# Performance work log

Measured on AMD Instinct MI355X. Metric: run time of the kernel, lower is better.

The kernel has to match this reference:

```python
import jax, jax.numpy as jnp
import numpy as np


def _build_skew(coeff, gate, left, right):
    # coeff: [B, r], gate: [B], left/right: [F, r]
    scaled_left = left[None, :, :] * coeff[:, None, :]          # [B, F, r]
    base = jnp.einsum('bfr,gr->bfg', scaled_left, right)         # [B, F, F]
    skew = base - jnp.swapaxes(base, -1, -2)
    return gate[:, None, None] * skew


def setup_inputs() -> dict:
    key = jax.random.key(0)
    ks = jax.random.split(key, 10)
    B, N, F, R = 8, 4096, 512, 16
    return {
        'x': jax.random.normal(ks[0], (B, N, F), dtype=jnp.float32),
        'coeff': jax.random.normal(ks[1], (B, R), dtype=jnp.float32),
        'gate': jax.random.uniform(ks[2], (B,), dtype=jnp.float32),
        'coeff_local': jax.random.normal(ks[3], (B, R), dtype=jnp.float32),
        'gate_local': jax.random.uniform(ks[4], (B,), dtype=jnp.float32),
        'comm_scale': jax.random.uniform(ks[5], (B,), dtype=jnp.float32),
        'left': jax.random.normal(ks[6], (F, R), dtype=jnp.float32) / np.sqrt(F),
        'right': jax.random.normal(ks[7], (F, R), dtype=jnp.float32) / np.sqrt(F),
        'left_local': jax.random.normal(ks[8], (F, R), dtype=jnp.float32) / np.sqrt(F),
        'right_local': jax.random.normal(ks[9], (F, R), dtype=jnp.float32) / np.sqrt(F),
    }


def reference(x, coeff, gate, coeff_local, gate_local, comm_scale,
              left, right, left_local, right_local):
    F_dim = left.shape[0]
    global_skew = _build_skew(coeff, gate, left, right)                  # [B, F, F]
    local_skew = _build_skew(coeff_local, gate_local, left_local, right_local)
    omega = 0.5 * (global_skew + local_skew)
    commutator = local_skew @ global_skew - global_skew @ local_skew
    omega = omega + comm_scale[:, None, None] * (commutator / 12.0)
    eye = jnp.eye(F_dim, dtype=jnp.float32)[None, :, :]
    # Cayley transform: (I - 0.5*Omega)^{-1} (I + 0.5*Omega)
    transform = jnp.linalg.solve(eye - 0.5 * omega, eye + 0.5 * omega)   # [B, F, F]
    mixed = jnp.einsum('bnd,bdh->bnh', x, transform)
    return mixed.astype(x.dtype)
```

## Files before the change

kernel.cpp:

```cpp
#include <hip/hip_runtime.h>

#define B_ 8
#define N_ 4096
#define F_ 512

typedef __attribute__((ext_vector_type(8))) short bf16x8;
typedef __attribute__((ext_vector_type(4))) float f32x4;

#define XPAD 524

__device__ __forceinline__ float Sval(const float* l, const float* r,
                                      const float* ll, const float* rl,
                                      int h, int e) {
    const int m = e >> 4, c = e & 15;
    const float* p = (m == 0) ? l : (m == 1) ? r : (m == 2) ? ll : rl;
    return p[h * 16 + c];
}

__device__ __forceinline__ float qval(const float* coeff, const float* coeff_l,
                                      int b, int j) {
    if (j < 16) return 1.f;
    if (j < 32) return coeff[b * 16 + (j - 16)];
    if (j < 48) return 1.f;
    return coeff_l[b * 16 + (j - 48)];
}

__device__ __forceinline__ float lane_bcast(float v, int lane) {
    return __int_as_float(__builtin_amdgcn_readlane(__float_as_int(v), lane));
}

__device__ __forceinline__ unsigned short bf16_rn(float x) {
    unsigned u = __float_as_uint(x);
    unsigned r = u + 0x7FFFu + ((u >> 16) & 1u);
    return (unsigned short)(r >> 16);
}

__device__ __forceinline__ void bf16_split(float x, short& hi, short& lo) {
    const unsigned short h = bf16_rn(x);
    const float hf = __uint_as_float(((unsigned)h) << 16);
    const unsigned short s = bf16_rn(x - hf);
    hi = (short)h; lo = (short)s;
}

__device__ __forceinline__ float b2f(unsigned short u) {
    return __uint_as_float(((unsigned)u) << 16);
}

__global__ __launch_bounds__(256) void k_prep(const float* l, const float* r,
                                              const float* ll, const float* rl,
                                              float* GS, unsigned short* Sf) {
    __shared__ float red[4][64];
    const int i = blockIdx.x;
    const int t = threadIdx.x;
    const int j = t & 63, seg = t >> 6;

    {
        const int ht = i >> 1, eh = i & 1;
        for (int idx = t; idx < 512; idx += 256) {
            const int lx = idx >> 3, ii = idx & 7;
            const int h = ht * 16 + (lx & 15);
            const int e = eh * 32 + ((lx >> 4) & 3) * 8 + ii;
            short hh, ss;
            bf16_split(Sval(l, r, ll, rl, h, e), hh, ss);
            Sf[(i * 2 + 0) * 512 + idx] = (unsigned short)hh;
            Sf[(i * 2 + 1) * 512 + idx] = (unsigned short)ss;
        }
    }

    float acc = 0.f;
    const int h0 = seg * 128;
    for (int h = h0; h < h0 + 128; ++h)
        acc += Sval(l, r, ll, rl, h, i) * Sval(l, r, ll, rl, h, j);
    red[seg][j] = acc;
    __syncthreads();
    if (t < 64) GS[i * 64 + t] = red[0][t] + red[1][t] + red[2][t] + red[3][t];
}

__global__ __launch_bounds__(256) void k_pre(const float* coeff, const float* gate,
                                             const float* coeff_l, const float* gate_l,
                                             const float* comm, const float* GS,
                                             float* Mws, float* CPws) {
    __shared__ float GST[4096];
    __shared__ float CPs[4096];
    __shared__ float ABs[2048];
    __shared__ float u1s[32], u2s[32];

    const int b = blockIdx.x, t = threadIdx.x;
    const int tx = t & 15, ty = t >> 4;
    const float g = gate[b], gl = gate_l[b];
    const float cs = comm[b] / 12.0f;

    if (t < 32) {
        u1s[t] = (t < 16) ? g * coeff[b * 16 + t] : -g;
        u2s[t] = (t < 16) ? gl * coeff_l[b * 16 + t] : -gl;
    }
    for (int idx = t; idx < 4096; idx += 256) {
        const int i = idx & 63, e = idx >> 6;
        GST[idx] = -0.5f * qval(coeff, coeff_l, b, i) * GS[(i ^ 16) * 64 + e];
    }
    __syncthreads();

    for (int idx = t; idx < 2048; idx += 256) {
        const int which = idx >> 10;
        const int i = (idx >> 5) & 31, j = idx & 31;
        float val;
        if (which == 0) {
            const int v2i = (i < 16) ? 48 + i : 16 + i;
            const float v2sc = (i < 16) ? 1.f : coeff_l[b * 16 + (i - 16)];
            val = v2sc * u1s[j] * GS[v2i * 64 + j];
        } else {
            const int v1i = (i < 16) ? 16 + i : i - 16;
            const float v1sc = (i < 16) ? 1.f : coeff[b * 16 + (i - 16)];
            val = v1sc * u2s[j] * GS[v1i * 64 + 32 + j];
        }
        ABs[idx] = val;
    }
    __syncthreads();

    for (int idx = t; idx < 4096; idx += 256) {
        const int e = idx >> 6, j = idx & 63;
        float val = 0.f;
        if (j < 32) {
            if (e == j) val += 0.5f * u1s[j];
            if (e >= 32) val += cs * u2s[e - 32] * ABs[(e - 32) * 32 + j];
        } else {
            const int jp = j - 32;
            if (e == 32 + jp) val += 0.5f * u2s[jp];
            if (e < 32) val -= cs * u1s[e] * ABs[1024 + e * 32 + jp];
        }
        CPs[idx] = val;
        CPws[b * 4096 + idx] = val;
    }
    __syncthreads();

    {
        const int i0 = ty * 4, m0 = tx * 4;
        float acc[4][4];
#pragma unroll
        for (int i = 0; i < 4; ++i)
#pragma unroll
            for (int j = 0; j < 4; ++j) acc[i][j] = 0.f;
        for (int e = 0; e < 64; ++e) {
            const float4 av = *reinterpret_cast<const float4*>(&GST[e * 64 + i0]);
            const float4 bv = *reinterpret_cast<const float4*>(&CPs[e * 64 + m0]);
            const float a[4] = {av.x, av.y, av.z, av.w};
            const float bb[4] = {bv.x, bv.y, bv.z, bv.w};
#pragma unroll
            for (int i = 0; i < 4; ++i)
#pragma unroll
                for (int j = 0; j < 4; ++j) acc[i][j] += a[i] * bb[j];
        }
#pragma unroll
        for (int i = 0; i < 4; ++i) {
            float4 o;
            o.x = acc[i][0] + (((i0 + i) == (m0 + 0)) ? 1.f : 0.f);
            o.y = acc[i][1] + (((i0 + i) == (m0 + 1)) ? 1.f : 0.f);
            o.z = acc[i][2] + (((i0 + i) == (m0 + 2)) ? 1.f : 0.f);
            o.w = acc[i][3] + (((i0 + i) == (m0 + 3)) ? 1.f : 0.f);
            *reinterpret_cast<float4*>(&Mws[b * 4096 + (i0 + i) * 64 + m0]) = o;
        }
    }
}

#define DO64(M, K) \
    M(0, K) M(1, K) M(2, K) M(3, K) M(4, K) M(5, K) M(6, K) M(7, K) \
    M(8, K) M(9, K) M(10, K) M(11, K) M(12, K) M(13, K) M(14, K) M(15, K) \
    M(16, K) M(17, K) M(18, K) M(19, K) M(20, K) M(21, K) M(22, K) M(23, K) \
    M(24, K) M(25, K) M(26, K) M(27, K) M(28, K) M(29, K) M(30, K) M(31, K) \
    M(32, K) M(33, K) M(34, K) M(35, K) M(36, K) M(37, K) M(38, K) M(39, K) \
    M(40, K) M(41, K) M(42, K) M(43, K) M(44, K) M(45, K) M(46, K) M(47, K) \
    M(48, K) M(49, K) M(50, K) M(51, K) M(52, K) M(53, K) M(54, K) M(55, K) \
    M(56, K) M(57, K) M(58, K) M(59, K) M(60, K) M(61, K) M(62, K) M(63, K)

#define GJ_LOAD(RR, K) a[RR] = Mws[base + (RR)*64 + t];
#define GJ_STORE(RR, K) Kws[base + (RR)*64 + t] = a[RR];

#define INV_SNAP(RR, G) if (ing) Msnap[(RR) * 8 + gl] = a[RR];

#define IGU(I, G, J) \
    if ((I) != (J)) { \
        const float f_ = lane_bcast(a[(G)*8 + (I)], (G)*8 + (J)); \
        a[(G)*8 + (I)] = __builtin_fmaf(-f_, akp[J], a[(G)*8 + (I)]); \
    }

#define IGS(G, J) { \
    const float dk = lane_bcast(a[(G)*8 + (J)], (G)*8 + (J)); \
    const float pinv = 1.0f / dk; \
    a[(G)*8 + (J)] = (t == ((G)*8 + (J))) ? pinv : a[(G)*8 + (J)] * pinv; \
    akp[J] = a[(G)*8 + (J)] + ((t == ((G)*8 + (J))) ? 1.0f : 0.0f); \
    IGU(0, G, J) IGU(1, G, J) IGU(2, G, J) IGU(3, G, J) \
    IGU(4, G, J) IGU(5, G, J) IGU(6, G, J) IGU(7, G, J) }

#define TRL(RR, G) \
    if (((RR) >> 3) != (G)) { \
        const float4 m0 = *reinterpret_cast<const float4*>(&Msnap[(RR) * 8]); \
        const float4 m1 = *reinterpret_cast<const float4*>(&Msnap[(RR) * 8 + 4]); \
        a[RR] = __builtin_fmaf(-m0.x, akp[0], a[RR]); \
        a[RR] = __builtin_fmaf(-m0.y, akp[1], a[RR]); \
        a[RR] = __builtin_fmaf(-m0.z, akp[2], a[RR]); \
        a[RR] = __builtin_fmaf(-m0.w, akp[3], a[RR]); \
        a[RR] = __builtin_fmaf(-m1.x, akp[4], a[RR]); \
        a[RR] = __builtin_fmaf(-m1.y, akp[5], a[RR]); \
        a[RR] = __builtin_fmaf(-m1.z, akp[6], a[RR]); \
        a[RR] = __builtin_fmaf(-m1.w, akp[7], a[RR]); \
    }

#define MACRO_STEP(G) { \
    float akp[8]; \
    const bool ing = ((t >> 3) == (G)); \
    DO64(INV_SNAP, G) \
    IGS(G, 0) IGS(G, 1) IGS(G, 2) IGS(G, 3) \
    IGS(G, 4) IGS(G, 5) IGS(G, 6) IGS(G, 7) \
    DO64(TRL, G) }

__global__ __launch_bounds__(64, 1) void k_inv(const float* Mws, float* Kws) {
    __shared__ float Msnap[512];
    const int b = blockIdx.x, t = threadIdx.x;
    const int base = b * 4096;
    const int gl = t & 7;
    float a[64];
    DO64(GJ_LOAD, 0)
    MACRO_STEP(0) MACRO_STEP(1) MACRO_STEP(2) MACRO_STEP(3)
    MACRO_STEP(4) MACRO_STEP(5) MACRO_STEP(6) MACRO_STEP(7)
    DO64(GJ_STORE, 0)
}

__global__ __launch_bounds__(256) void k_sepost(const float* coeff, const float* coeff_l,
                                                const float* l, const float* r,
                                                const float* ll, const float* rl,
                                                const float* Mws, const float* CPws,
                                                const float* Kws, unsigned short* SEf) {
    __shared__ float smem[20480];
    float* Ms  = smem;
    float* CPs = smem + 4096;
    float* Ks  = smem + 8192;
    float* Tds = smem + 12288;
    float* Tas = smem + 16384;
    float* Es  = smem;
    float* Ss  = smem + 4096;
    float* SEs = smem + 8320;

    const int b = blockIdx.y, hc = blockIdx.x, t = threadIdx.x;
    const int tx = t & 15, ty = t >> 4;

    for (int idx = t; idx < 4096; idx += 256) {
        Ms[idx] = Mws[b * 4096 + idx];
        CPs[idx] = CPws[b * 4096 + idx];
        Ks[idx] = Kws[b * 4096 + idx];
    }
    __syncthreads();

    {
        const int i0 = ty * 4, j0 = tx * 4;
        float accd[4][4], acca[4][4];
#pragma unroll
        for (int i = 0; i < 4; ++i)
#pragma unroll
            for (int j = 0; j < 4; ++j) { accd[i][j] = 0.f; acca[i][j] = 0.f; }
        for (int q = 0; q < 64; ++q) {
            const float4 bv = *reinterpret_cast<const float4*>(&Ks[q * 64 + j0]);
            const float bb[4] = {bv.x, bv.y, bv.z, bv.w};
            float ad[4], aa[4];
#pragma unroll
            for (int i = 0; i < 4; ++i) {
                ad[i] = CPs[(i0 + i) * 64 + q];
                aa[i] = Ms[(i0 + i) * 64 + q];
            }
#pragma unroll
            for (int i = 0; i < 4; ++i)
#pragma unroll
                for (int j = 0; j < 4; ++j) {
                    accd[i][j] += ad[i] * bb[j];
                    acca[i][j] += aa[i] * bb[j];
                }
        }
        __syncthreads();
#pragma unroll
        for (int i = 0; i < 4; ++i)
#pragma unroll
            for (int j = 0; j < 4; ++j) {
                Tds[(i0 + i) * 64 + j0 + j] = accd[i][j];
                Tas[(i0 + i) * 64 + j0 + j] = acca[i][j];
            }
    }
    __syncthreads();

    {
        const int e0 = ty * 4, c0 = tx * 4;
        float acc[4][4];
#pragma unroll
        for (int i = 0; i < 4; ++i)
#pragma unroll
            for (int j = 0; j < 4; ++j) acc[i][j] = 0.f;
        for (int q = 0; q < 64; ++q) {
            const float4 bv = *reinterpret_cast<const float4*>(&Tas[q * 64 + c0]);
            const float bb[4] = {bv.x, bv.y, bv.z, bv.w};
            float a[4];
#pragma unroll
            for (int i = 0; i < 4; ++i) a[i] = Tds[(e0 + i) * 64 + q];
#pragma unroll
            for (int i = 0; i < 4; ++i)
#pragma unroll
                for (int j = 0; j < 4; ++j) acc[i][j] += a[i] * bb[j];
        }
        float qv[4];
#pragma unroll
        for (int j = 0; j < 4; ++j) qv[j] = qval(coeff, coeff_l, b, c0 + j);
#pragma unroll
        for (int i = 0; i < 4; ++i) {
            float4 o;
            o.x = qv[0] * (2.f * Tds[(e0 + i) * 64 + c0 + 0] - acc[i][0]);
            o.y = qv[1] * (2.f * Tds[(e0 + i) * 64 + c0 + 1] - acc[i][1]);
            o.z = qv[2] * (2.f * Tds[(e0 + i) * 64 + c0 + 2] - acc[i][2]);
            o.w = qv[3] * (2.f * Tds[(e0 + i) * 64 + c0 + 3] - acc[i][3]);
            *reinterpret_cast<float4*>(&Es[(e0 + i) * 64 + (c0 ^ 16)]) = o;
        }
        for (int idx = t; idx < 4096; idx += 256) {
            const int hl_ = idx >> 6, e = idx & 63;
            Ss[hl_ * 66 + e] = Sval(l, r, ll, rl, hc * 64 + hl_, e);
        }
    }
    __syncthreads();

    {
        const int h = t >> 2;
        const int mg = (t & 3) * 16;
        float acc[16];
#pragma unroll
        for (int q = 0; q < 16; ++q) acc[q] = 0.f;
#pragma unroll 4
        for (int e = 0; e < 64; ++e) {
            const float s = Ss[h * 66 + e];
            const float* Er = Es + e * 64 + mg;
#pragma unroll
            for (int q = 0; q < 16; ++q) acc[q] += s * Er[q];
        }
        __syncthreads();
#pragma unroll
        for (int q = 0; q < 16; ++q) SEs[h * 65 + mg + q] = acc[q];
    }
    __syncthreads();

    unsigned short* outp = SEf + (size_t)b * 65536 + hc * 8192;
#pragma unroll
    for (int it = 0; it < 4; ++it) {
        const int widx0 = it * 2048 + t * 8;
        const int fl = widx0 >> 10;
        const int hl = (widx0 >> 9) & 1;
        const int lx = (widx0 >> 3) & 63;
        const int m = (fl & 3) * 16 + (lx & 15);
        const int hb = (fl >> 2) * 32 + ((lx >> 4) & 3) * 8;
        unsigned short wv[8];
#pragma unroll
        for (int i = 0; i < 8; ++i) {
            short hh, ss;
            bf16_split(SEs[(hb + i) * 65 + m], hh, ss);
            wv[i] = hl ? (unsigned short)ss : (unsigned short)hh;
        }
        uint4 pk;
        pk.x = (unsigned)wv[0] | ((unsigned)wv[1] << 16);
        pk.y = (unsigned)wv[2] | ((unsigned)wv[3] << 16);
        pk.z = (unsigned)wv[4] | ((unsigned)wv[5] << 16);
        pk.w = (unsigned)wv[6] | ((unsigned)wv[7] << 16);
        *reinterpret_cast<uint4*>(outp + widx0) = pk;
    }
}

__global__ __launch_bounds__(256, 2) void k_mix(const float* x,
                                                const unsigned short* SEf,
                                                const unsigned short* Sf,
                                                float* out) {
    __shared__ unsigned short xh[32 * XPAD];
    __shared__ unsigned short xl[32 * XPAD];
    __shared__ float Zs[32 * 68];
    const int b = blockIdx.y;
    const int r0 = blockIdx.x * 32;
    const int t = threadIdx.x;
    const int w = t >> 6;
    const int l = t & 63;
    const int lm = l & 15;
    const int lk = (l >> 4) * 8;
    const int rw = w & 1, cw = w >> 1;
    const float* xb = x + (size_t)b * N_ * F_;
    float* outb = out + (size_t)b * N_ * F_;
    const unsigned short* sef = SEf + (size_t)b * 65536;

#pragma unroll 4
    for (int it = 0; it < 16; ++it) {
        const int idx = it * 256 + t;
        const int row = idx >> 7, c4 = (idx & 127) * 4;
        const float4 v = *reinterpret_cast<const float4*>(
            xb + (size_t)(r0 + row) * F_ + c4);
        ushort4 hs, ls;
        short hh, ss;
        bf16_split(v.x, hh, ss); hs.x = (unsigned short)hh; ls.x = (unsigned short)ss;
        bf16_split(v.y, hh, ss); hs.y = (unsigned short)hh; ls.y = (unsigned short)ss;
        bf16_split(v.z, hh, ss); hs.z = (unsigned short)hh; ls.z = (unsigned short)ss;
        bf16_split(v.w, hh, ss); hs.w = (unsigned short)hh; ls.w = (unsigned short)ss;
        *reinterpret_cast<ushort4*>(&xh[row * XPAD + c4]) = hs;
        *reinterpret_cast<ushort4*>(&xl[row * XPAD + c4]) = ls;
    }
    __syncthreads();

    f32x4 ahh0 = {0.f, 0.f, 0.f, 0.f}, alh0 = ahh0, ahl0 = ahh0;
    f32x4 ahh1 = ahh0, alh1 = ahh0, ahl1 = ahh0;
    const unsigned short* xhr = xh + (16 * rw + lm) * XPAD;
    const unsigned short* xlr = xl + (16 * rw + lm) * XPAD;
#pragma unroll 4
    for (int kk = 0; kk < 16; ++kk) {
        const int k0 = kk * 32 + lk;
        const bf16x8 ah = *reinterpret_cast<const bf16x8*>(xhr + k0);
        const bf16x8 al = *reinterpret_cast<const bf16x8*>(xlr + k0);
        const int o0 = (kk * 4 + 2 * cw) * 1024 + l * 8;
        const bf16x8 bh0 = *reinterpret_cast<const bf16x8*>(sef + o0);
        const bf16x8 bl0 = *reinterpret_cast<const bf16x8*>(sef + o0 + 512);
        const bf16x8 bh1 = *reinterpret_cast<const bf16x8*>(sef + o0 + 1024);
        const bf16x8 bl1 = *reinterpret_cast<const bf16x8*>(sef + o0 + 1536);
        ahh0 = __builtin_amdgcn_mfma_f32_16x16x32_bf16(ah, bh0, ahh0, 0, 0, 0);
        alh0 = __builtin_amdgcn_mfma_f32_16x16x32_bf16(al, bh0, alh0, 0, 0, 0);
        ahl0 = __builtin_amdgcn_mfma_f32_16x16x32_bf16(ah, bl0, ahl0, 0, 0, 0);
        ahh1 = __builtin_amdgcn_mfma_f32_16x16x32_bf16(ah, bh1, ahh1, 0, 0, 0);
        alh1 = __builtin_amdgcn_mfma_f32_16x16x32_bf16(al, bh1, alh1, 0, 0, 0);
        ahl1 = __builtin_amdgcn_mfma_f32_16x16x32_bf16(ah, bl1, ahl1, 0, 0, 0);
    }
#pragma unroll
    for (int r = 0; r < 4; ++r) {
        const int zr = (16 * rw + (l >> 4) * 4 + r) * 68 + 32 * cw;
        Zs[zr + lm] = ahh0[r] + alh0[r] + ahl0[r];
        Zs[zr + 16 + lm] = ahh1[r] + alh1[r] + ahl1[r];
    }
    __syncthreads();

    bf16x8 zh0, zl0, zh1, zl1;
    {
        const float* zrow = &Zs[(16 * rw + lm) * 68];
#pragma unroll
        for (int i = 0; i < 8; ++i) {
            short hh, ss;
            bf16_split(zrow[lk + i], hh, ss);
            zh0[i] = hh; zl0[i] = ss;
            bf16_split(zrow[32 + lk + i], hh, ss);
            zh1[i] = hh; zl1[i] = ss;
        }
    }
    const int lrow0 = 16 * rw + (l >> 4) * 4;
    const int orow0 = r0 + lrow0;
#pragma unroll 2
    for (int j2 = 0; j2 < 16; ++j2) {
        const int ht = cw * 16 + j2;
        const int h0 = ht * 16 + lm;
        f32x4 ca = {0.f, 0.f, 0.f, 0.f};
        f32x4 cb;
#pragma unroll
        for (int r = 0; r < 4; ++r) {
            const int la = (lrow0 + r) * XPAD + h0;
            cb[r] = b2f(xh[la]) + b2f(xl[la]);
        }
        const int fb = ht * 2048 + l * 8;
        const bf16x8 bh0 = *reinterpret_cast<const bf16x8*>(Sf + fb);
        const bf16x8 bl0 = *reinterpret_cast<const bf16x8*>(Sf + fb + 512);
        const bf16x8 bh1 = *reinterpret_cast<const bf16x8*>(Sf + fb + 1024);
        const bf16x8 bl1 = *reinterpret_cast<const bf16x8*>(Sf + fb + 1536);
        ca = __builtin_amdgcn_mfma_f32_16x16x32_bf16(zh0, bh0, ca, 0, 0, 0);
        ca = __builtin_amdgcn_mfma_f32_16x16x32_bf16(zl0, bh0, ca, 0, 0, 0);
        ca = __builtin_amdgcn_mfma_f32_16x16x32_bf16(zh0, bl0, ca, 0, 0, 0);
        cb = __builtin_amdgcn_mfma_f32_16x16x32_bf16(zh1, bh1, cb, 0, 0, 0);
        cb = __builtin_amdgcn_mfma_f32_16x16x32_bf16(zl1, bh1, cb, 0, 0, 0);
        cb = __builtin_amdgcn_mfma_f32_16x16x32_bf16(zh1, bl1, cb, 0, 0, 0);
#pragma unroll
        for (int r = 0; r < 4; ++r)
            outb[(size_t)(orow0 + r) * F_ + h0] = ca[r] + cb[r];
    }
}

extern "C" void kernel_launch(void* const* d_in, const int* in_sizes, int n_in,
                              void* d_out, int out_size, void* d_ws, size_t ws_size,
                              hipStream_t stream) {
    (void)in_sizes; (void)n_in; (void)out_size; (void)ws_size;
    const float* x       = (const float*)d_in[0];
    const float* coeff   = (const float*)d_in[1];
    const float* gate    = (const float*)d_in[2];
    const float* coeff_l = (const float*)d_in[3];
    const float* gate_l  = (const float*)d_in[4];
    const float* comm    = (const float*)d_in[5];
    const float* l       = (const float*)d_in[6];
    const float* r       = (const float*)d_in[7];
    const float* ll      = (const float*)d_in[8];
    const float* rl      = (const float*)d_in[9];

    char* wsb = (char*)d_ws;
    float* GS   = (float*)(wsb);
    unsigned short* SEf = (unsigned short*)(wsb + 147456);
    unsigned short* Sf  = (unsigned short*)(wsb + 1196032);
    float* Mws  = (float*)(wsb + 1327104);
    float* CPws = (float*)(wsb + 1458176);
    float* Kws  = (float*)(wsb + 1589248);
    float* out = (float*)d_out;

    k_prep<<<dim3(64), dim3(256), 0, stream>>>(l, r, ll, rl, GS, Sf);
    k_pre<<<dim3(8), dim3(256), 0, stream>>>(coeff, gate, coeff_l, gate_l, comm, GS,
                                             Mws, CPws);
    k_inv<<<dim3(8), dim3(64), 0, stream>>>(Mws, Kws);
    k_sepost<<<dim3(8, 8), dim3(256), 0, stream>>>(coeff, coeff_l, l, r, ll, rl,
                                                   Mws, CPws, Kws, SEf);
    k_mix<<<dim3(128, 8), dim3(256), 0, stream>>>(x, SEf, Sf, out);
}
```

Measured before the change: 112.2 us.

## Fuse pre, inverse and post-solve kernels into one per-batch solve kernel

Merges k_pre, k_inv and k_sepost into a single k_solve kernel per batch, keeping the 64x64 intermediates (M, CP, K) in shared memory instead of round-tripping through global workspace. The Gauss-Jordan inverse now runs across four waves with pivot rows shared via LDS, where before it ran on a single wave. The post stage now loops over all eight h-chunks inside one block, where before it was spread over 64 blocks. This removes two launches and the global traffic between them, but the SE product is now serialized on 8 blocks, so per-block work grows.

```diff
diff --git a/kernel.cpp b/kernel.cpp
--- a/kernel.cpp
+++ b/kernel.cpp
@@ -76,14 +76,26 @@
     if (t < 64) GS[i * 64 + t] = red[0][t] + red[1][t] + red[2][t] + red[3][t];
 }
 
-__global__ __launch_bounds__(256) void k_pre(const float* coeff, const float* gate,
-                                             const float* coeff_l, const float* gate_l,
-                                             const float* comm, const float* GS,
-                                             float* Mws, float* CPws) {
-    __shared__ float GST[4096];
-    __shared__ float CPs[4096];
-    __shared__ float ABs[2048];
-    __shared__ float u1s[32], u2s[32];
+__global__ __launch_bounds__(256) void k_solve(const float* coeff, const float* gate,
+                                               const float* coeff_l, const float* gate_l,
+                                               const float* comm, const float* GSg,
+                                               const float* l, const float* r,
+                                               const float* ll, const float* rl,
+                                               unsigned short* SEf) {
+    __shared__ float smem[17024];
+    float* GST = smem;
+    float* CPs = smem + 4096;
+    float* ABs = smem + 8192;
+    float* Ms  = smem + 8192;
+    float* Ks  = smem + 12288;
+    float* Tds = smem;
+    float* Tas = smem + 8192;
+    float* Es  = smem + 4096;
+    float* SEs = smem + 8192;
+    float* Ss  = smem + 12352;
+    float* akp_lds = smem + 16384;
+    float* u1s = smem + 16896;
+    float* u2s = smem + 16928;
 
     const int b = blockIdx.x, t = threadIdx.x;
     const int tx = t & 15, ty = t >> 4;
@@ -96,7 +108,7 @@
     }
     for (int idx = t; idx < 4096; idx += 256) {
         const int i = idx & 63, e = idx >> 6;
-        GST[idx] = -0.5f * qval(coeff, coeff_l, b, i) * GS[(i ^ 16) * 64 + e];
+        GST[idx] = -0.5f * qval(coeff, coeff_l, b, i) * GSg[(i ^ 16) * 64 + e];
     }
     __syncthreads();
 
@@ -107,11 +119,11 @@
         if (which == 0) {
             const int v2i = (i < 16) ? 48 + i : 16 + i;
             const float v2sc = (i < 16) ? 1.f : coeff_l[b * 16 + (i - 16)];
-            val = v2sc * u1s[j] * GS[v2i * 64 + j];
+            val = v2sc * u1s[j] * GSg[v2i * 64 + j];
         } else {
             const int v1i = (i < 16) ? 16 + i : i - 16;
             const float v1sc = (i < 16) ? 1.f : coeff[b * 16 + (i - 16)];
-            val = v1sc * u2s[j] * GS[v1i * 64 + 32 + j];
+            val = v1sc * u2s[j] * GSg[v1i * 64 + 32 + j];
         }
         ABs[idx] = val;
     }
@@ -129,7 +141,6 @@
             if (e < 32) val -= cs * u1s[e] * ABs[1024 + e * 32 + jp];
         }
         CPs[idx] = val;
-        CPws[b * 4096 + idx] = val;
     }
     __syncthreads();
 
@@ -151,102 +162,71 @@
                 for (int j = 0; j < 4; ++j) acc[i][j] += a[i] * bb[j];
         }
 #pragma unroll
-        for (int i = 0; i < 4; ++i) {
-            float4 o;
-            o.x = acc[i][0] + (((i0 + i) == (m0 + 0)) ? 1.f : 0.f);
-            o.y = acc[i][1] + (((i0 + i) == (m0 + 1)) ? 1.f : 0.f);
-            o.z = acc[i][2] + (((i0 + i) == (m0 + 2)) ? 1.f : 0.f);
-            o.w = acc[i][3] + (((i0 + i) == (m0 + 3)) ? 1.f : 0.f);
-            *reinterpret_cast<float4*>(&Mws[b * 4096 + (i0 + i) * 64 + m0]) = o;
-        }
-    }
-}
-
-#define DO64(M, K) \
-    M(0, K) M(1, K) M(2, K) M(3, K) M(4, K) M(5, K) M(6, K) M(7, K) \
-    M(8, K) M(9, K) M(10, K) M(11, K) M(12, K) M(13, K) M(14, K) M(15, K) \
-    M(16, K) M(17, K) M(18, K) M(19, K) M(20, K) M(21, K) M(22, K) M(23, K) \
-    M(24, K) M(25, K) M(26, K) M(27, K) M(28, K) M(29, K) M(30, K) M(31, K) \
-    M(32, K) M(33, K) M(34, K) M(35, K) M(36, K) M(37, K) M(38, K) M(39, K) \
-    M(40, K) M(41, K) M(42, K) M(43, K) M(44, K) M(45, K) M(46, K) M(47, K) \
-    M(48, K) M(49, K) M(50, K) M(51, K) M(52, K) M(53, K) M(54, K) M(55, K) \
-    M(56, K) M(57, K) M(58, K) M(59, K) M(60, K) M(61, K) M(62, K) M(63, K)
-
-#define GJ_LOAD(RR, K) a[RR] = Mws[base + (RR)*64 + t];
-#define GJ_STORE(RR, K) Kws[base + (RR)*64 + t] = a[RR];
-
-#define INV_SNAP(RR, G) if (ing) Msnap[(RR) * 8 + gl] = a[RR];
-
-#define IGU(I, G, J) \
-    if ((I) != (J)) { \
-        const float f_ = lane_bcast(a[(G)*8 + (I)], (G)*8 + (J)); \
-        a[(G)*8 + (I)] = __builtin_fmaf(-f_, akp[J], a[(G)*8 + (I)]); \
-    }
-
-#define IGS(G, J) { \
-    const float dk = lane_bcast(a[(G)*8 + (J)], (G)*8 + (J)); \
-    const float pinv = 1.0f / dk; \
-    a[(G)*8 + (J)] = (t == ((G)*8 + (J))) ? pinv : a[(G)*8 + (J)] * pinv; \
-    akp[J] = a[(G)*8 + (J)] + ((t == ((G)*8 + (J))) ? 1.0f : 0.0f); \
-    IGU(0, G, J) IGU(1, G, J) IGU(2, G, J) IGU(3, G, J) \
-    IGU(4, G, J) IGU(5, G, J) IGU(6, G, J) IGU(7, G, J) }
-
-#define TRL(RR, G) \
-    if (((RR) >> 3) != (G)) { \
-        const float4 m0 = *reinterpret_cast<const float4*>(&Msnap[(RR) * 8]); \
-        const float4 m1 = *reinterpret_cast<const float4*>(&Msnap[(RR) * 8 + 4]); \
-        a[RR] = __builtin_fmaf(-m0.x, akp[0], a[RR]); \
-        a[RR] = __builtin_fmaf(-m0.y, akp[1], a[RR]); \
-        a[RR] = __builtin_fmaf(-m0.z, akp[2], a[RR]); \
-        a[RR] = __builtin_fmaf(-m0.w, akp[3], a[RR]); \
-        a[RR] = __builtin_fmaf(-m1.x, akp[4], a[RR]); \
-        a[RR] = __builtin_fmaf(-m1.y, akp[5], a[RR]); \
-        a[RR] = __builtin_fmaf(-m1.z, akp[6], a[RR]); \
-        a[RR] = __builtin_fmaf(-m1.w, akp[7], a[RR]); \
-    }
-
-#define MACRO_STEP(G) { \
-    float akp[8]; \
-    const bool ing = ((t >> 3) == (G)); \
-    DO64(INV_SNAP, G) \
-    IGS(G, 0) IGS(G, 1) IGS(G, 2) IGS(G, 3) \
-    IGS(G, 4) IGS(G, 5) IGS(G, 6) IGS(G, 7) \
-    DO64(TRL, G) }
-
-__global__ __launch_bounds__(64, 1) void k_inv(const float* Mws, float* Kws) {
-    __shared__ float Msnap[512];
-    const int b = blockIdx.x, t = threadIdx.x;
-    const int base = b * 4096;
-    const int gl = t & 7;
-    float a[64];
-    DO64(GJ_LOAD, 0)
-    MACRO_STEP(0) MACRO_STEP(1) MACRO_STEP(2) MACRO_STEP(3)
-    MACRO_STEP(4) MACRO_STEP(5) MACRO_STEP(6) MACRO_STEP(7)
-    DO64(GJ_STORE, 0)
-}
-
-__global__ __launch_bounds__(256) void k_sepost(const float* coeff, const float* coeff_l,
-                                                const float* l, const float* r,
-                                                const float* ll, const float* rl,
-                                                const float* Mws, const float* CPws,
-                                                const float* Kws, unsigned short* SEf) {
-    __shared__ float smem[20480];
-    float* Ms  = smem;
-    float* CPs = smem + 4096;
-    float* Ks  = smem + 8192;
-    float* Tds = smem + 12288;
-    float* Tas = smem + 16384;
-    float* Es  = smem;
-    float* Ss  = smem + 4096;
-    float* SEs = smem + 8320;
-
-    const int b = blockIdx.y, hc = blockIdx.x, t = threadIdx.x;
-    const int tx = t & 15, ty = t >> 4;
-
-    for (int idx = t; idx < 4096; idx += 256) {
-        Ms[idx] = Mws[b * 4096 + idx];
-        CPs[idx] = CPws[b * 4096 + idx];
-        Ks[idx] = Kws[b * 4096 + idx];
+        for (int i = 0; i < 4; ++i)
+#pragma unroll
+            for (int j = 0; j < 4; ++j)
+                Ms[(i0 + i) * 64 + m0 + j] =
+                    acc[i][j] + (((i0 + i) == (m0 + j)) ? 1.f : 0.f);
+    }
+    __syncthreads();
+
+    {
+        const int wv = t >> 6, ln = t & 63;
+        float a[16];
+#pragma unroll
+        for (int i = 0; i < 16; ++i) a[i] = Ms[(wv * 16 + i) * 64 + ln];
+#pragma unroll
+        for (int G = 0; G < 8; ++G) {
+            __syncthreads();
+            float akpr[8];
+            const int ow = G >> 1;
+            if (wv == ow) {
+#pragma unroll
+                for (int J = 0; J < 8; ++J) {
+                    const int Bq = (G & 1) * 8;
+                    const float dk = lane_bcast(a[Bq + J], 8 * G + J);
+                    const float pinv = 1.0f / dk;
+                    a[Bq + J] = (ln == 8 * G + J) ? pinv : a[Bq + J] * pinv;
+                    akpr[J] = a[Bq + J] + ((ln == 8 * G + J) ? 1.0f : 0.0f);
+                    akp_lds[J * 64 + ln] = akpr[J];
+#pragma unroll
+                    for (int I = 0; I < 8; ++I) {
+                        if (I != J) {
+                            const float f = lane_bcast(a[Bq + I], 8 * G + J);
+                            a[Bq + I] = __builtin_fmaf(-f, akpr[J], a[Bq + I]);
+                        }
+                    }
+                }
+            }
+            __syncthreads();
+            if (wv != ow) {
+#pragma unroll
+                for (int j = 0; j < 8; ++j) akpr[j] = akp_lds[j * 64 + ln];
+            }
+#pragma unroll
+            for (int i = 0; i < 16; ++i) {
+                if (((wv * 16 + i) >> 3) != G) {
+                    const float f0 = lane_bcast(a[i], 8 * G + 0);
+                    const float f1 = lane_bcast(a[i], 8 * G + 1);
+                    const float f2 = lane_bcast(a[i], 8 * G + 2);
+                    const float f3 = lane_bcast(a[i], 8 * G + 3);
+                    const float f4 = lane_bcast(a[i], 8 * G + 4);
+                    const float f5 = lane_bcast(a[i], 8 * G + 5);
+                    const float f6 = lane_bcast(a[i], 8 * G + 6);
+                    const float f7 = lane_bcast(a[i], 8 * G + 7);
+                    a[i] = __builtin_fmaf(-f0, akpr[0], a[i]);
+                    a[i] = __builtin_fmaf(-f1, akpr[1], a[i]);
+                    a[i] = __builtin_fmaf(-f2, akpr[2], a[i]);
+                    a[i] = __builtin_fmaf(-f3, akpr[3], a[i]);
+                    a[i] = __builtin_fmaf(-f4, akpr[4], a[i]);
+                    a[i] = __builtin_fmaf(-f5, akpr[5], a[i]);
+                    a[i] = __builtin_fmaf(-f6, akpr[6], a[i]);
+                    a[i] = __builtin_fmaf(-f7, akpr[7], a[i]);
+                }
+            }
+        }
+#pragma unroll
+        for (int i = 0; i < 16; ++i) Ks[(wv * 16 + i) * 64 + ln] = a[i];
     }
     __syncthreads();
 
@@ -315,54 +295,56 @@
             o.w = qv[3] * (2.f * Tds[(e0 + i) * 64 + c0 + 3] - acc[i][3]);
             *reinterpret_cast<float4*>(&Es[(e0 + i) * 64 + (c0 ^ 16)]) = o;
         }
+    }
+    __syncthreads();
+
+    for (int hc = 0; hc < 8; ++hc) {
         for (int idx = t; idx < 4096; idx += 256) {
             const int hl_ = idx >> 6, e = idx & 63;
             Ss[hl_ * 66 + e] = Sval(l, r, ll, rl, hc * 64 + hl_, e);
         }
-    }
-    __syncthreads();
-
-    {
-        const int h = t >> 2;
-        const int mg = (t & 3) * 16;
-        float acc[16];
-#pragma unroll
-        for (int q = 0; q < 16; ++q) acc[q] = 0.f;
+        __syncthreads();
+        {
+            const int h = t >> 2;
+            const int mg = (t & 3) * 16;
+            float acc[16];
+#pragma unroll
+            for (int q = 0; q < 16; ++q) acc[q] = 0.f;
 #pragma unroll 4
-        for (int e = 0; e < 64; ++e) {
-            const float s = Ss[h * 66 + e];
-            const float* Er = Es + e * 64 + mg;
-#pragma unroll
-            for (int q = 0; q < 16; ++q) acc[q] += s * Er[q];
+            for (int e = 0; e < 64; ++e) {
+                const float s = Ss[h * 66 + e];
+                const float* Er = Es + e * 64 + mg;
+#pragma unroll
+                for (int q = 0; q < 16; ++q) acc[q] += s * Er[q];
+            }
+#pragma unroll
+            for (int q = 0; q < 16; ++q) SEs[h * 65 + mg + q] = acc[q];
         }
         __syncthreads();
-#pragma unroll
-        for (int q = 0; q < 16; ++q) SEs[h * 65 + mg + q] = acc[q];
-    }
-    __syncthreads();
-
-    unsigned short* outp = SEf + (size_t)b * 65536 + hc * 8192;
-#pragma unroll
-    for (int it = 0; it < 4; ++it) {
-        const int widx0 = it * 2048 + t * 8;
-        const int fl = widx0 >> 10;
-        const int hl = (widx0 >> 9) & 1;
-        const int lx = (widx0 >> 3) & 63;
-        const int m = (fl & 3) * 16 + (lx & 15);
-        const int hb = (fl >> 2) * 32 + ((lx >> 4) & 3) * 8;
-        unsigned short wv[8];
-#pragma unroll
-        for (int i = 0; i < 8; ++i) {
-            short hh, ss;
-            bf16_split(SEs[(hb + i) * 65 + m], hh, ss);
-            wv[i] = hl ? (unsigned short)ss : (unsigned short)hh;
-        }
-        uint4 pk;
-        pk.x = (unsigned)wv[0] | ((unsigned)wv[1] << 16);
-        pk.y = (unsigned)wv[2] | ((unsigned)wv[3] << 16);
-        pk.z = (unsigned)wv[4] | ((unsigned)wv[5] << 16);
-        pk.w = (unsigned)wv[6] | ((unsigned)wv[7] << 16);
-        *reinterpret_cast<uint4*>(outp + widx0) = pk;
+        unsigned short* outp = SEf + (size_t)b * 65536 + hc * 8192;
+#pragma unroll
+        for (int it = 0; it < 4; ++it) {
+            const int widx0 = it * 2048 + t * 8;
+            const int fl = widx0 >> 10;
+            const int hl = (widx0 >> 9) & 1;
+            const int lx = (widx0 >> 3) & 63;
+            const int m = (fl & 3) * 16 + (lx & 15);
+            const int hb = (fl >> 2) * 32 + ((lx >> 4) & 3) * 8;
+            unsigned short wv[8];
+#pragma unroll
+            for (int i = 0; i < 8; ++i) {
+                short hh, ss;
+                bf16_split(SEs[(hb + i) * 65 + m], hh, ss);
+                wv[i] = hl ? (unsigned short)ss : (unsigned short)hh;
+            }
+            uint4 pk;
+            pk.x = (unsigned)wv[0] | ((unsigned)wv[1] << 16);
+            pk.y = (unsigned)wv[2] | ((unsigned)wv[3] << 16);
+            pk.z = (unsigned)wv[4] | ((unsigned)wv[5] << 16);
+            pk.w = (unsigned)wv[6] | ((unsigned)wv[7] << 16);
+            *reinterpret_cast<uint4*>(outp + widx0) = pk;
+        }
+        __syncthreads();
     }
 }
 
@@ -492,16 +474,10 @@
     float* GS   = (float*)(wsb);
     unsigned short* SEf = (unsigned short*)(wsb + 147456);
     unsigned short* Sf  = (unsigned short*)(wsb + 1196032);
-    float* Mws  = (float*)(wsb + 1327104);
-    float* CPws = (float*)(wsb + 1458176);
-    float* Kws  = (float*)(wsb + 1589248);
     float* out = (float*)d_out;
 
     k_prep<<<dim3(64), dim3(256), 0, stream>>>(l, r, ll, rl, GS, Sf);
-    k_pre<<<dim3(8), dim3(256), 0, stream>>>(coeff, gate, coeff_l, gate_l, comm, GS,
-                                             Mws, CPws);
-    k_inv<<<dim3(8), dim3(64), 0, stream>>>(Mws, Kws);
-    k_sepost<<<dim3(8, 8), dim3(256), 0, stream>>>(coeff, coeff_l, l, r, ll, rl,
-                                                   Mws, CPws, Kws, SEf);
+    k_solve<<<dim3(8), dim3(256), 0, stream>>>(coeff, gate, coeff_l, gate_l, comm, GS,
+                                               l, r, ll, rl, SEf);
     k_mix<<<dim3(128, 8), dim3(256), 0, stream>>>(x, SEf, Sf, out);
 }
```

Measured after the change: 121.5 us. 8.3% more time.
